# Kernel tuning notes

Measured on AMD Instinct MI355X. Metric: run time of the kernel, lower is better.

Reference implementation:

```python
import jax, jax.numpy as jnp
import numpy as np

N, E, HD, L, A = 50000, 600000, 128, 4, 50
EIN = 3 * HD + 1  # edge MLP input: [h_row, h_col, dist, lam_e]


def _p(k, shape, scale=0.05):
    return (scale * jax.random.normal(k, shape)).astype(jnp.float32)


def setup_inputs() -> dict:
    key = jax.random.key(0)
    ks = jax.random.split(key, 24)
    inp = {
        "z": jax.random.randint(ks[0], (N,), 0, A),
        "pos": jax.random.normal(ks[1], (N, 3), dtype=jnp.float32),
        "edge_index": jax.random.randint(ks[2], (2, E), 0, N),
        "lam": jax.random.uniform(ks[3], (), dtype=jnp.float32),
        "atom_embed": _p(ks[4], (A, HD), 1.0),
        "lam_w": _p(ks[5], (1, HD)),
        "lam_b": _p(ks[6], (HD,)),
        "edge_w1": _p(ks[7], (L, EIN, HD)),
        "edge_b1": jnp.zeros((L, HD), jnp.float32),
        "edge_w2": _p(ks[8], (L, HD, HD)),
        "edge_b2": jnp.zeros((L, HD), jnp.float32),
        "node_w1": _p(ks[9], (L, 2 * HD, HD)),
        "node_b1": jnp.zeros((L, HD), jnp.float32),
        "node_w2": _p(ks[10], (L, HD, HD)),
        "node_b2": jnp.zeros((L, HD), jnp.float32),
        "ln_g": jnp.ones((L, HD), jnp.float32),
        "ln_b": jnp.zeros((L, HD), jnp.float32),
        "head_w1": _p(ks[11], (HD, HD)),
        "head_b1": jnp.zeros((HD,), jnp.float32),
        "head_w2": _p(ks[12], (HD, 1)),
        "head_b2": jnp.zeros((1,), jnp.float32),
    }
    return inp


def _layernorm(x, g, b, eps=1e-5):
    mu = jnp.mean(x, -1, keepdims=True)
    var = jnp.mean(jnp.square(x - mu), -1, keepdims=True)
    return (x - mu) * jax.lax.rsqrt(var + eps) * g + b


def reference(z, pos, edge_index, lam, atom_embed, lam_w, lam_b,
              edge_w1, edge_b1, edge_w2, edge_b2,
              node_w1, node_b1, node_w2, node_b2, ln_g, ln_b,
              head_w1, head_b1, head_w2, head_b2):
    h = atom_embed[z]                                  # [N, HD]
    # lambda_embed(lam.expand(N,1)): same vector for every node
    lam_vec = lam * lam_w[0] + lam_b                    # [HD]
    lam_feat = jnp.broadcast_to(lam_vec, (h.shape[0], HD))
    h = h + lam_feat
    row, col = edge_index[0], edge_index[1]
    diff = pos[row] - pos[col]                          # [E, 3] (constant over layers)
    dist = jnp.sqrt(jnp.sum(diff * diff, -1, keepdims=True) + 1e-8)  # [E,1]
    lam_e = lam_feat[row]                               # [E, HD]
    for i in range(L):
        ein = jnp.concatenate([h[row], h[col], dist, lam_e], -1)      # [E, 3*HD+1]
        m = jax.nn.silu(ein @ edge_w1[i] + edge_b1[i])
        m = jax.nn.silu(m @ edge_w2[i] + edge_b2[i])                  # [E, HD]
        agg = jnp.zeros_like(h).at[row].add(m)                        # scatter-add
        u = jax.nn.silu(jnp.concatenate([h, agg], -1) @ node_w1[i] + node_b1[i])
        u = u @ node_w2[i] + node_b2[i]
        h = _layernorm(h + u, ln_g[i], ln_b[i])
    pooled = jnp.mean(h, 0, keepdims=True)              # [1, HD]
    out = jax.nn.silu(pooled @ head_w1 + head_b1) @ head_w2 + head_b2  # [1, 1]
    return out
```

## Files before the change

kernel.cpp:

```cpp
#include <hip/hip_runtime.h>
#include <cstdint>
#include <cstddef>

#define HD 128
#define NLAYER 4
#define EINDIM 385

typedef _Float16 f16x8 __attribute__((ext_vector_type(8)));
typedef _Float16 f16x4 __attribute__((ext_vector_type(4)));
typedef float f32x4 __attribute__((ext_vector_type(4)));

__device__ __forceinline__ float silu_f(float x) {
    float e = __expf(-x);
    return x * __builtin_amdgcn_rcpf(1.f + e);
}

__device__ __forceinline__ void lds_barrier() {
    asm volatile("s_waitcnt lgkmcnt(0)" ::: "memory");
    __builtin_amdgcn_s_barrier();
}

__global__ __launch_bounds__(128) void k_init(const float* __restrict__ lam_p,
                                              const float* __restrict__ lam_w,
                                              const float* __restrict__ lam_b,
                                              const float* __restrict__ edge_w1,
                                              const float* __restrict__ edge_b1,
                                              float* __restrict__ lam_vec,
                                              float* __restrict__ c1) {
    __shared__ float sl[HD];
    const int j = threadIdx.x;
    const int l = blockIdx.x;
    float lam = lam_p[0];
    float v = lam * lam_w[j] + lam_b[j];
    sl[j] = v;
    if (l == 0) lam_vec[j] = v;
    __syncthreads();
    float acc = edge_b1[l * HD + j];
    const float* w = edge_w1 + ((size_t)l * EINDIM + 257) * HD + j;
#pragma unroll 8
    for (int k = 0; k < HD; k++) acc = fmaf(sl[k], w[(size_t)k * HD], acc);
    c1[l * HD + j] = acc;
}

__global__ void k_prep(const float* __restrict__ ew1, const float* __restrict__ ew2,
                       const float* __restrict__ nw1, const float* __restrict__ nw2,
                       _Float16* __restrict__ W1te, _Float16* __restrict__ W2te,
                       _Float16* __restrict__ W1tn, _Float16* __restrict__ W2tn,
                       float* __restrict__ wd) {
    int t = blockIdx.x * 256 + threadIdx.x;
    if (t < NLAYER * 128 * 256) {
        int l = t >> 15, r = t & 32767, j = r >> 8, k = r & 255;
        W1te[t] = (_Float16)ew1[((size_t)l * EINDIM + k) * HD + j];
        return;
    }
    t -= NLAYER * 128 * 256;
    if (t < NLAYER * 128 * 256) {
        int l = t >> 15, r = t & 32767, j = r >> 8, k = r & 255;
        W1tn[t] = (_Float16)nw1[((size_t)l * 256 + k) * HD + j];
        return;
    }
    t -= NLAYER * 128 * 256;
    if (t < NLAYER * 128 * 128) {
        int l = t >> 14, r = t & 16383, j = r >> 7, k = r & 127;
        W2te[t] = (_Float16)ew2[((size_t)l * 128 + k) * HD + j];
        return;
    }
    t -= NLAYER * 128 * 128;
    if (t < NLAYER * 128 * 128) {
        int l = t >> 14, r = t & 16383, j = r >> 7, k = r & 127;
        W2tn[t] = (_Float16)nw2[((size_t)l * 128 + k) * HD + j];
        return;
    }
    t -= NLAYER * 128 * 128;
    if (t < NLAYER * 128) {
        int l = t >> 7, j = t & 127;
        wd[t] = ew1[((size_t)l * EINDIM + 256) * HD + j];
    }
}

__global__ void k_embed(const int* __restrict__ z,
                        const float* __restrict__ atom_embed,
                        const float* __restrict__ lam_vec,
                        float* __restrict__ h, _Float16* __restrict__ hh, int n4) {
    int i = blockIdx.x * 256 + threadIdx.x;
    if (i >= n4) return;
    int n = i >> 5, q = i & 31;
    int a = z[n];
    float4 e = *(const float4*)&atom_embed[(size_t)a * HD + q * 4];
    float4 lv = *(const float4*)&lam_vec[q * 4];
    e.x += lv.x; e.y += lv.y; e.z += lv.z; e.w += lv.w;
    *(float4*)&h[(size_t)n * HD + q * 4] = e;
    f16x4 hv;
    hv[0] = (_Float16)e.x; hv[1] = (_Float16)e.y;
    hv[2] = (_Float16)e.z; hv[3] = (_Float16)e.w;
    *(f16x4*)&hh[(size_t)n * HD + q * 4] = hv;
}

__global__ void k_zero(float4* __restrict__ p, int n4) {
    for (int i = blockIdx.x * 256 + threadIdx.x; i < n4; i += gridDim.x * 256)
        p[i] = make_float4(0.f, 0.f, 0.f, 0.f);
}

__global__ void k_hist(const int* __restrict__ ei, int* __restrict__ deg, int E) {
    int e = blockIdx.x * 256 + threadIdx.x;
    if (e < E) atomicAdd(&deg[ei[e]], 1);
}

__global__ __launch_bounds__(1024) void k_scan(const int* __restrict__ deg,
                                               int* __restrict__ cursor, int N) {
    __shared__ int part[1024];
    int t = threadIdx.x;
    int chunk = (N + 1023) >> 10;
    int s0 = t * chunk, s1 = s0 + chunk;
    if (s1 > N) s1 = N;
    int s = 0;
    for (int i = s0; i < s1; i++) s += deg[i];
    part[t] = s;
    __syncthreads();
    for (int d = 1; d < 1024; d <<= 1) {
        int v = (t >= d) ? part[t - d] : 0;
        __syncthreads();
        part[t] += v;
        __syncthreads();
    }
    int base = (t == 0) ? 0 : part[t - 1];
    for (int i = s0; i < s1; i++) {
        cursor[i] = base;
        base += deg[i];
    }
}

__global__ void k_scatter(const int* __restrict__ ei, int* __restrict__ cursor,
                          int* __restrict__ perm, int E) {
    int e = blockIdx.x * 256 + threadIdx.x;
    if (e < E) {
        int p = atomicAdd(&cursor[ei[e]], 1);
        perm[p] = e;
    }
}

__global__ void k_apply(const int* __restrict__ perm, const int* __restrict__ ei,
                        const float* __restrict__ pos,
                        int* __restrict__ rowS, int* __restrict__ colS,
                        float* __restrict__ distS, int E, int Epad) {
    int i = blockIdx.x * 256 + threadIdx.x;
    if (i >= Epad) return;
    if (i < E) {
        int e = perm[i];
        int r = ei[e], c = ei[E + e];
        rowS[i] = r; colS[i] = c;
        float dx = pos[r * 3 + 0] - pos[c * 3 + 0];
        float dy = pos[r * 3 + 1] - pos[c * 3 + 1];
        float dz = pos[r * 3 + 2] - pos[c * 3 + 2];
        distS[i] = sqrtf(dx * dx + dy * dy + dz * dz + 1e-8f);
    } else {
        rowS[i] = -1; colS[i] = 0; distS[i] = 0.f;
    }
}

__global__ void k_mask(const int* __restrict__ rowS,
                       unsigned long long* __restrict__ maskBuf, int Epad) {
    int i = blockIdx.x * 256 + threadIdx.x;
    if (i >= Epad) return;
    bool pred = (i + 1 >= Epad) ? true : (rowS[i] != rowS[i + 1]);
    unsigned long long m = __ballot(pred);
    if ((i & 63) == 0) maskBuf[i >> 6] = m;
}

__global__ __launch_bounds__(512, 4) void k_edge_mfma(
    const _Float16* __restrict__ hh,
    const int* __restrict__ rowS, const int* __restrict__ colS,
    const float* __restrict__ distS,
    const unsigned long long* __restrict__ maskBuf,
    int Epad, int ntiles, int tpb,
    const _Float16* __restrict__ W1t,
    const _Float16* __restrict__ W2t,
    const float* __restrict__ wd, const float* __restrict__ c1,
    const float* __restrict__ b2,
    float* __restrict__ agg) {
    __shared__ __align__(16) _Float16 shA[64 * 264];
    __shared__ __align__(16) _Float16 shM[64 * 136];
    __shared__ int shRow2[2][64];
    __shared__ float shD2[2][64];
    __shared__ float shWd[HD], shC1[HD], shB2[HD];

    const int tid = threadIdx.x;
    const int w = tid >> 6, l = tid & 63;
    const int lg = l >> 4, lr = l & 15;
    const int col = w * 16 + lr;

    f16x8 w1f[8], w2f[4];
#pragma unroll
    for (int s = 0; s < 8; s++)
        w1f[s] = *(const f16x8*)(W1t + (size_t)col * 256 + s * 32 + lg * 8);
#pragma unroll
    for (int s = 0; s < 4; s++)
        w2f[s] = *(const f16x8*)(W2t + (size_t)col * 128 + s * 32 + lg * 8);
    if (tid < 128) { shWd[tid] = wd[tid]; shC1[tid] = c1[tid]; }
    else if (tid < 256) shB2[tid - 128] = b2[tid - 128];

    const int t0 = blockIdx.x * tpb;
    int t1 = t0 + tpb; if (t1 > ntiles) t1 = ntiles;
    if (t0 >= t1) return;

    f16x8 vA[4];
    int rv = -1; float dv = 0.f;

    {
        const int e0 = t0 * 64;
        if (tid < 64) { rv = rowS[e0 + tid]; dv = distS[e0 + tid]; }
#pragma unroll
        for (int it = 0; it < 4; it++) {
            int flat = tid + it * 512;
            int e = flat >> 5, c = flat & 31;
            int idx = (c < 16) ? rowS[e0 + e] : colS[e0 + e];
            if (idx < 0) idx = 0;
            int cc = (c < 16) ? c : (c - 16);
            vA[it] = *(const f16x8*)(hh + (size_t)idx * HD + cc * 8);
        }
    }
    __syncthreads();

    for (int t = t0; t < t1; t++) {
        const int pb = t & 1;
        const unsigned long long bmCur = maskBuf[t];
        const unsigned long long bmPrev = (t > 0) ? maskBuf[t - 1] : ~0ull;

#pragma unroll
        for (int it = 0; it < 4; it++) {
            int flat = tid + it * 512;
            int e = flat >> 5, c = flat & 31;
            *(f16x8*)&shA[e * 264 + c * 8] = vA[it];
        }
        if (tid < 64) { shRow2[pb][tid] = rv; shD2[pb][tid] = dv; }

        {
            int tn = t + 1; if (tn > ntiles - 1) tn = ntiles - 1;
            const int e0n = tn * 64;
#pragma unroll
            for (int it = 0; it < 4; it++) {
                int flat = tid + it * 512;
                int e = flat >> 5, c = flat & 31;
                int idx = (c < 16) ? rowS[e0n + e] : colS[e0n + e];
                if (idx < 0) idx = 0;
                int cc = (c < 16) ? c : (c - 16);
                vA[it] = *(const f16x8*)(hh + (size_t)idx * HD + cc * 8);
            }
            if (tid < 64) { rv = rowS[e0n + tid]; dv = distS[e0n + tid]; }
        }

        lds_barrier();

        f32x4 acc[4];
#pragma unroll
        for (int rf = 0; rf < 4; rf++) acc[rf] = (f32x4){0.f, 0.f, 0.f, 0.f};

#pragma unroll
        for (int s = 0; s < 8; s++) {
#pragma unroll
            for (int rf = 0; rf < 4; rf++) {
                f16x8 a = *(const f16x8*)&shA[(rf * 16 + lr) * 264 + s * 32 + lg * 8];
                acc[rf] = __builtin_amdgcn_mfma_f32_16x16x32_f16(a, w1f[s], acc[rf], 0, 0, 0);
            }
        }
#pragma unroll
        for (int rf = 0; rf < 4; rf++) {
#pragma unroll
            for (int r = 0; r < 4; r++) {
                int row = rf * 16 + lg * 4 + r;
                float x = acc[rf][r] + shD2[pb][row] * shWd[col] + shC1[col];
                shM[row * 136 + col] = (_Float16)silu_f(x);
            }
            acc[rf] = (f32x4){0.f, 0.f, 0.f, 0.f};
        }
        lds_barrier();

#pragma unroll
        for (int s = 0; s < 4; s++) {
#pragma unroll
            for (int rf = 0; rf < 4; rf++) {
                f16x8 a = *(const f16x8*)&shM[(rf * 16 + lr) * 136 + s * 32 + lg * 8];
                acc[rf] = __builtin_amdgcn_mfma_f32_16x16x32_f16(a, w2f[s], acc[rf], 0, 0, 0);
            }
        }
        lds_barrier();

#pragma unroll
        for (int rf = 0; rf < 4; rf++) {
#pragma unroll
            for (int r = 0; r < 4; r++) {
                int row = rf * 16 + lg * 4 + r;
                shM[row * 136 + col] = (_Float16)silu_f(acc[rf][r] + shB2[col]);
            }
        }
        lds_barrier();

        {
            const int scol = tid & 127, quarter = tid >> 7;
            const int i0 = quarter << 4;
            const unsigned int mh = (unsigned int)(bmCur >> i0) & 0xFFFFu;
            bool open = (quarter == 0) ? !((bmPrev >> 63) & 1ull)
                                       : !((bmCur >> (i0 - 1)) & 1ull);
            float s = 0.f;
#pragma unroll
            for (int ib = 0; ib < 4; ib++) {
                const int i = i0 + ib * 4;
                float v0 = (float)shM[(i + 0) * 136 + scol];
                float v1 = (float)shM[(i + 1) * 136 + scol];
                float v2 = (float)shM[(i + 2) * 136 + scol];
                float v3 = (float)shM[(i + 3) * 136 + scol];
#pragma unroll
                for (int q = 0; q < 4; q++) {
                    s += (q == 0) ? v0 : (q == 1) ? v1 : (q == 2) ? v2 : v3;
                    if (mh & (1u << (ib * 4 + q))) {
                        int rc = shRow2[pb][i + q];
                        if (rc >= 0) {
                            if (open) atomicAdd(&agg[(size_t)rc * HD + scol], s);
                            else      agg[(size_t)rc * HD + scol] = s;
                        }
                        s = 0.f;
                        open = false;
                    }
                }
            }
            if (!((mh >> 15) & 1u)) {
                int rc = shRow2[pb][i0 + 15];
                if (rc >= 0) atomicAdd(&agg[(size_t)rc * HD + scol], s);
            }
        }
    }
}

__global__ __launch_bounds__(256, 3) void k_node_mfma(
    const _Float16* __restrict__ hh_in, float* __restrict__ agg, int N,
    int ntiles, int tpb,
    const _Float16* __restrict__ W1t,
    const _Float16* __restrict__ W2t,
    const float* __restrict__ b1, const float* __restrict__ b2,
    const float* __restrict__ lng, const float* __restrict__ lnb,
    float* __restrict__ h, _Float16* __restrict__ hh_out) {
    __shared__ __align__(16) _Float16 shA[64 * 264];
    __shared__ __align__(16) _Float16 shM[64 * 136];
    __shared__ float shB1[HD], shB2[HD], shG[HD], shBt[HD];

    const int tid = threadIdx.x;
    const int w = tid >> 6, l = tid & 63;
    const int lg = l >> 4, lr = l & 15;

    f16x8 w1f[2][8], w2f[2][4];
#pragma unroll
    for (int cf = 0; cf < 2; cf++) {
        const int col = w * 32 + cf * 16 + lr;
#pragma unroll
        for (int s = 0; s < 8; s++)
            w1f[cf][s] = *(const f16x8*)(W1t + (size_t)col * 256 + s * 32 + lg * 8);
#pragma unroll
        for (int s = 0; s < 4; s++)
            w2f[cf][s] = *(const f16x8*)(W2t + (size_t)col * 128 + s * 32 + lg * 8);
    }
    if (tid < 128) { shB1[tid] = b1[tid]; shB2[tid] = b2[tid]; }
    else { shG[tid - 128] = lng[tid - 128]; shBt[tid - 128] = lnb[tid - 128]; }
    __syncthreads();

    int t1 = blockIdx.x * tpb + tpb;
    if (t1 > ntiles) t1 = ntiles;
    for (int t = blockIdx.x * tpb; t < t1; t++) {
        const int n0 = t * 64;

#pragma unroll
        for (int it = 0; it < 8; it++) {
            int flat = tid + it * 256;
            int e = flat >> 5, c = flat & 31;
            int n = n0 + e;
            f16x8 v = {};
            if (n < N) {
                if (c < 16) {
                    v = *(const f16x8*)(hh_in + (size_t)n * HD + c * 8);
                } else {
                    float* s = agg + (size_t)n * HD + (c - 16) * 8;
                    float4 v0 = *(const float4*)s;
                    float4 v1 = *(const float4*)(s + 4);
                    v[0] = (_Float16)v0.x; v[1] = (_Float16)v0.y;
                    v[2] = (_Float16)v0.z; v[3] = (_Float16)v0.w;
                    v[4] = (_Float16)v1.x; v[5] = (_Float16)v1.y;
                    v[6] = (_Float16)v1.z; v[7] = (_Float16)v1.w;
                    float4 z4 = make_float4(0.f, 0.f, 0.f, 0.f);
                    *(float4*)s = z4;
                    *(float4*)(s + 4) = z4;
                }
            }
            *(f16x8*)&shA[e * 264 + c * 8] = v;
        }
        lds_barrier();

        f32x4 acc[4][2];
#pragma unroll
        for (int rf = 0; rf < 4; rf++)
#pragma unroll
            for (int cf = 0; cf < 2; cf++) acc[rf][cf] = (f32x4){0.f, 0.f, 0.f, 0.f};

#pragma unroll
        for (int s = 0; s < 8; s++) {
#pragma unroll
            for (int rf = 0; rf < 4; rf++) {
                f16x8 a = *(const f16x8*)&shA[(rf * 16 + lr) * 264 + s * 32 + lg * 8];
                acc[rf][0] = __builtin_amdgcn_mfma_f32_16x16x32_f16(a, w1f[0][s], acc[rf][0], 0, 0, 0);
                acc[rf][1] = __builtin_amdgcn_mfma_f32_16x16x32_f16(a, w1f[1][s], acc[rf][1], 0, 0, 0);
            }
        }
#pragma unroll
        for (int rf = 0; rf < 4; rf++)
#pragma unroll
            for (int cf = 0; cf < 2; cf++) {
                const int col = w * 32 + cf * 16 + lr;
#pragma unroll
                for (int r = 0; r < 4; r++) {
                    int row = rf * 16 + lg * 4 + r;
                    shM[row * 136 + col] = (_Float16)silu_f(acc[rf][cf][r] + shB1[col]);
                }
            }
        lds_barrier();

        f32x4 acc2[4][2];
#pragma unroll
        for (int rf = 0; rf < 4; rf++)
#pragma unroll
            for (int cf = 0; cf < 2; cf++) acc2[rf][cf] = (f32x4){0.f, 0.f, 0.f, 0.f};

#pragma unroll
        for (int s = 0; s < 4; s++) {
#pragma unroll
            for (int rf = 0; rf < 4; rf++) {
                f16x8 a = *(const f16x8*)&shM[(rf * 16 + lr) * 136 + s * 32 + lg * 8];
                acc2[rf][0] = __builtin_amdgcn_mfma_f32_16x16x32_f16(a, w2f[0][s], acc2[rf][0], 0, 0, 0);
                acc2[rf][1] = __builtin_amdgcn_mfma_f32_16x16x32_f16(a, w2f[1][s], acc2[rf][1], 0, 0, 0);
            }
        }
        lds_barrier();

#pragma unroll
        for (int rf = 0; rf < 4; rf++)
#pragma unroll
            for (int cf = 0; cf < 2; cf++) {
                const int col = w * 32 + cf * 16 + lr;
#pragma unroll
                for (int r = 0; r < 4; r++) {
                    int row = rf * 16 + lg * 4 + r;
                    shM[row * 136 + col] = (_Float16)(acc2[rf][cf][r] + shB2[col]);
                }
            }
        lds_barrier();

        {
            int row = tid >> 2, q = tid & 3, n = n0 + row;
            float s = 0.f, ss = 0.f;
            if (n < N) {
#pragma unroll
                for (int j = 0; j < 8; j++) {
                    float4 hv = *(const float4*)&h[(size_t)n * HD + q * 32 + j * 4];
                    int cb = q * 32 + j * 4;
                    f16x4 uv = *(const f16x4*)&shM[row * 136 + cb];
                    float x0 = (float)uv[0] + hv.x;
                    float x1 = (float)uv[1] + hv.y;
                    float x2 = (float)uv[2] + hv.z;
                    float x3 = (float)uv[3] + hv.w;
                    s += x0 + x1 + x2 + x3;
                    ss += x0 * x0 + x1 * x1 + x2 * x2 + x3 * x3;
                }
            }
            s += __shfl_xor(s, 1);  s += __shfl_xor(s, 2);
            ss += __shfl_xor(ss, 1); ss += __shfl_xor(ss, 2);
            float mean = s * (1.f / 128.f);
            float var = ss * (1.f / 128.f) - mean * mean;
            float rstd = rsqrtf(var + 1e-5f);
            if (n < N) {
#pragma unroll
                for (int j = 0; j < 8; j++) {
                    float4 hv = *(const float4*)&h[(size_t)n * HD + q * 32 + j * 4];
                    int cb = q * 32 + j * 4;
                    f16x4 uv = *(const f16x4*)&shM[row * 136 + cb];
                    float4 y;
                    y.x = ((float)uv[0] + hv.x - mean) * rstd * shG[cb + 0] + shBt[cb + 0];
                    y.y = ((float)uv[1] + hv.y - mean) * rstd * shG[cb + 1] + shBt[cb + 1];
                    y.z = ((float)uv[2] + hv.z - mean) * rstd * shG[cb + 2] + shBt[cb + 2];
                    y.w = ((float)uv[3] + hv.w - mean) * rstd * shG[cb + 3] + shBt[cb + 3];
                    *(float4*)&h[(size_t)n * HD + cb] = y;
                    f16x4 yh;
                    yh[0] = (_Float16)y.x; yh[1] = (_Float16)y.y;
                    yh[2] = (_Float16)y.z; yh[3] = (_Float16)y.w;
                    *(f16x4*)&hh_out[(size_t)n * HD + cb] = yh;
                }
            }
        }
    }
}

__global__ __launch_bounds__(256) void k_pool1(const float* __restrict__ h,
                                               float* __restrict__ partial,
                                               int N, int RPB) {
    int bk = blockIdx.x, t = threadIdx.x;
    int j = t & 127, half = t >> 7;
    float s = 0.f;
    int rend = (bk + 1) * RPB; if (rend > N) rend = N;
    for (int r = bk * RPB + half; r < rend; r += 2) s += h[(size_t)r * HD + j];
    __shared__ float sh[256];
    sh[t] = s;
    __syncthreads();
    if (t < 128) partial[bk * HD + j] = sh[t] + sh[t + 128];
}

__global__ __launch_bounds__(128) void k_head(const float* __restrict__ partial,
                                              int nPart, int N,
                                              const float* __restrict__ hw1,
                                              const float* __restrict__ hb1,
                                              const float* __restrict__ hw2,
                                              const float* __restrict__ hb2,
                                              float* __restrict__ out) {
    __shared__ float pooled[HD];
    __shared__ float t1[HD];
    int j = threadIdx.x;
    double s = 0.0;
    for (int bk = 0; bk < nPart; bk++) s += (double)partial[bk * HD + j];
    pooled[j] = (float)(s / (double)N);
    __syncthreads();
    float acc = hb1[j];
    for (int k = 0; k < HD; k++) acc = fmaf(pooled[k], hw1[k * HD + j], acc);
    t1[j] = silu_f(acc) * hw2[j];
    __syncthreads();
    if (j < 64) t1[j] += t1[j + 64];
    __syncthreads();
    if (j < 64) {
        float v = t1[j];
#pragma unroll
        for (int o = 32; o > 0; o >>= 1) v += __shfl_xor(v, o);
        if (j == 0) out[0] = v + hb2[0];
    }
}

extern "C" void kernel_launch(void* const* d_in, const int* in_sizes, int n_in,
                              void* d_out, int out_size, void* d_ws, size_t ws_size,
                              hipStream_t stream) {
    const int* z      = (const int*)d_in[0];
    const float* pos  = (const float*)d_in[1];
    const int* ei     = (const int*)d_in[2];
    const float* lam  = (const float*)d_in[3];
    const float* aemb = (const float*)d_in[4];
    const float* lamw = (const float*)d_in[5];
    const float* lamb = (const float*)d_in[6];
    const float* ew1  = (const float*)d_in[7];
    const float* eb1  = (const float*)d_in[8];
    const float* ew2  = (const float*)d_in[9];
    const float* eb2  = (const float*)d_in[10];
    const float* nw1  = (const float*)d_in[11];
    const float* nb1  = (const float*)d_in[12];
    const float* nw2  = (const float*)d_in[13];
    const float* nb2  = (const float*)d_in[14];
    const float* lng  = (const float*)d_in[15];
    const float* lnb  = (const float*)d_in[16];
    const float* hw1  = (const float*)d_in[17];
    const float* hb1  = (const float*)d_in[18];
    const float* hw2  = (const float*)d_in[19];
    const float* hb2  = (const float*)d_in[20];

    const int N = in_sizes[0];
    const int E = in_sizes[2] / 2;
    const int etiles = (E + 63) / 64;
    const int Epad = etiles * 64;
    const int ntilesN = (N + 63) / 64;

    char* ws = (char*)d_ws;
    size_t off = 0;
    auto alloc = [&](size_t bytes) { void* p = ws + off; off += (bytes + 255) & ~(size_t)255; return p; };
    float* h        = (float*)alloc((size_t)N * HD * 4);
    float* agg      = (float*)alloc((size_t)N * HD * 4);
    _Float16* hh    = (_Float16*)alloc((size_t)N * HD * 2);
    int* deg        = (int*)alloc((size_t)N * 4);
    int* cursor     = (int*)alloc((size_t)N * 4);
    int* perm       = (int*)alloc((size_t)E * 4);
    int* rowS       = (int*)alloc((size_t)Epad * 4);
    int* colS       = (int*)alloc((size_t)Epad * 4);
    float* distS    = (float*)alloc((size_t)Epad * 4);
    unsigned long long* maskBuf = (unsigned long long*)alloc((size_t)etiles * 8);
    float* lamv     = (float*)alloc(HD * 4);
    float* c1       = (float*)alloc(NLAYER * HD * 4);
    float* wd       = (float*)alloc(NLAYER * HD * 4);
    float* part     = (float*)alloc(256 * HD * 4);
    _Float16* W1te  = (_Float16*)alloc((size_t)NLAYER * 128 * 256 * 2);
    _Float16* W1tn  = (_Float16*)alloc((size_t)NLAYER * 128 * 256 * 2);
    _Float16* W2te  = (_Float16*)alloc((size_t)NLAYER * 128 * 128 * 2);
    _Float16* W2tn  = (_Float16*)alloc((size_t)NLAYER * 128 * 128 * 2);

    k_init<<<NLAYER, 128, 0, stream>>>(lam, lamw, lamb, ew1, eb1, lamv, c1);
    int prepTot = NLAYER * 128 * 256 * 2 + NLAYER * 128 * 128 * 2 + NLAYER * 128;
    k_prep<<<(prepTot + 255) / 256, 256, 0, stream>>>(ew1, ew2, nw1, nw2,
                                                      W1te, W2te, W1tn, W2tn, wd);
    int n4 = N * 32;
    k_embed<<<(n4 + 255) / 256, 256, 0, stream>>>(z, aemb, lamv, h, hh, n4);

    k_zero<<<64, 256, 0, stream>>>((float4*)deg, (N + 3) / 4);
    k_hist<<<(E + 255) / 256, 256, 0, stream>>>(ei, deg, E);
    k_scan<<<1, 1024, 0, stream>>>(deg, cursor, N);
    k_scatter<<<(E + 255) / 256, 256, 0, stream>>>(ei, cursor, perm, E);
    k_apply<<<(Epad + 255) / 256, 256, 0, stream>>>(perm, ei, pos, rowS, colS, distS, E, Epad);
    k_mask<<<(Epad + 255) / 256, 256, 0, stream>>>(rowS, maskBuf, Epad);

    int zero4 = N * (HD / 4);
    k_zero<<<2048, 256, 0, stream>>>((float4*)agg, zero4);

    const int egrid = (etiles < 512) ? etiles : 512;
    const int etpb = (etiles + egrid - 1) / egrid;
    const int ngrid = (ntilesN + 1) / 2;
    for (int l = 0; l < NLAYER; l++) {
        k_edge_mfma<<<egrid, 512, 0, stream>>>(hh, rowS, colS, distS, maskBuf,
            Epad, etiles, etpb,
            W1te + (size_t)l * 128 * 256, W2te + (size_t)l * 128 * 128,
            wd + l * HD, c1 + l * HD, eb2 + l * HD, agg);
        k_node_mfma<<<ngrid, 256, 0, stream>>>(hh, agg, N, ntilesN, 2,
            W1tn + (size_t)l * 128 * 256, W2tn + (size_t)l * 128 * 128,
            nb1 + l * HD, nb2 + l * HD, lng + l * HD, lnb + l * HD, h, hh);
    }
    int RPB = (N + 255) / 256;
    k_pool1<<<256, 256, 0, stream>>>(h, part, N, RPB);
    k_head<<<1, 128, 0, stream>>>(part, 256, N, hw1, hb1, hw2, hb2, (float*)d_out);
}
```

Baseline: 958.9 us.

## Factor first edge-MLP layer into per-node projections gathered per edge

The first edge linear layer is split by linearity: each node's h is projected once through the row and col halves of W1 in a new per-node MFMA kernel (P, Q), and the edge kernel gathers P[row]+Q[col] and adds the dist and lambda terms before SiLU. This replaces the per-edge 256-wide GEMM with a 128-wide node GEMM over far fewer nodes, and removes one LDS staging buffer and barrier from the edge loop. It adds an extra kernel launch per layer and an extra write/read of two N×128 half buffers, and the pre-activation sum is now done in fp16-rounded pieces, which slightly changes precision.

```diff
diff --git a/kernel.cpp b/kernel.cpp
--- a/kernel.cpp
+++ b/kernel.cpp
@@ -26,7 +26,8 @@
                                               const float* __restrict__ edge_w1,
                                               const float* __restrict__ edge_b1,
                                               float* __restrict__ lam_vec,
-                                              float* __restrict__ c1) {
+                                              float* __restrict__ c1,
+                                              _Float16* __restrict__ c1h) {
     __shared__ float sl[HD];
     const int j = threadIdx.x;
     const int l = blockIdx.x;
@@ -40,13 +41,14 @@
 #pragma unroll 8
     for (int k = 0; k < HD; k++) acc = fmaf(sl[k], w[(size_t)k * HD], acc);
     c1[l * HD + j] = acc;
+    c1h[l * HD + j] = (_Float16)acc;
 }
 
 __global__ void k_prep(const float* __restrict__ ew1, const float* __restrict__ ew2,
                        const float* __restrict__ nw1, const float* __restrict__ nw2,
                        _Float16* __restrict__ W1te, _Float16* __restrict__ W2te,
                        _Float16* __restrict__ W1tn, _Float16* __restrict__ W2tn,
-                       float* __restrict__ wd) {
+                       float* __restrict__ wd, _Float16* __restrict__ wdh) {
     int t = blockIdx.x * 256 + threadIdx.x;
     if (t < NLAYER * 128 * 256) {
         int l = t >> 15, r = t & 32767, j = r >> 8, k = r & 255;
@@ -74,7 +76,9 @@
     t -= NLAYER * 128 * 128;
     if (t < NLAYER * 128) {
         int l = t >> 7, j = t & 127;
-        wd[t] = ew1[((size_t)l * EINDIM + 256) * HD + j];
+        float v = ew1[((size_t)l * EINDIM + 256) * HD + j];
+        wd[t] = v;
+        wdh[t] = (_Float16)v;
     }
 }
 
@@ -167,86 +171,143 @@
     if ((i & 63) == 0) maskBuf[i >> 6] = m;
 }
 
+__global__ __launch_bounds__(512, 4) void k_pq(
+    const _Float16* __restrict__ hh, int N,
+    const _Float16* __restrict__ W1t,
+    _Float16* __restrict__ Ph, _Float16* __restrict__ Qh) {
+    __shared__ __align__(16) _Float16 shH[64 * 136];
+    const int tid = threadIdx.x;
+    const int w = tid >> 6, l = tid & 63;
+    const int lg = l >> 4, lr = l & 15;
+    const int col = w * 16 + lr;
+
+    f16x8 w1a[4], w1b[4];
+#pragma unroll
+    for (int s = 0; s < 4; s++) {
+        w1a[s] = *(const f16x8*)(W1t + (size_t)col * 256 + s * 32 + lg * 8);
+        w1b[s] = *(const f16x8*)(W1t + (size_t)col * 256 + 128 + s * 32 + lg * 8);
+    }
+    const int n0 = blockIdx.x * 64;
+#pragma unroll
+    for (int it = 0; it < 2; it++) {
+        int flat = tid + it * 512;
+        int e = flat >> 4, c = flat & 15;
+        int n = n0 + e;
+        f16x8 v = {};
+        if (n < N) v = *(const f16x8*)(hh + (size_t)n * HD + c * 8);
+        *(f16x8*)&shH[e * 136 + c * 8] = v;
+    }
+    __syncthreads();
+
+    f32x4 aP[4], aQ[4];
+#pragma unroll
+    for (int rf = 0; rf < 4; rf++) { aP[rf] = (f32x4){0,0,0,0}; aQ[rf] = (f32x4){0,0,0,0}; }
+#pragma unroll
+    for (int s = 0; s < 4; s++) {
+#pragma unroll
+        for (int rf = 0; rf < 4; rf++) {
+            f16x8 a = *(const f16x8*)&shH[(rf * 16 + lr) * 136 + s * 32 + lg * 8];
+            aP[rf] = __builtin_amdgcn_mfma_f32_16x16x32_f16(a, w1a[s], aP[rf], 0, 0, 0);
+            aQ[rf] = __builtin_amdgcn_mfma_f32_16x16x32_f16(a, w1b[s], aQ[rf], 0, 0, 0);
+        }
+    }
+#pragma unroll
+    for (int rf = 0; rf < 4; rf++) {
+#pragma unroll
+        for (int r = 0; r < 4; r++) {
+            int n = n0 + rf * 16 + lg * 4 + r;
+            if (n < N) {
+                Ph[(size_t)n * HD + col] = (_Float16)aP[rf][r];
+                Qh[(size_t)n * HD + col] = (_Float16)aQ[rf][r];
+            }
+        }
+    }
+}
+
 __global__ __launch_bounds__(512, 4) void k_edge_mfma(
-    const _Float16* __restrict__ hh,
+    const _Float16* __restrict__ Ph, const _Float16* __restrict__ Qh,
     const int* __restrict__ rowS, const int* __restrict__ colS,
     const float* __restrict__ distS,
     const unsigned long long* __restrict__ maskBuf,
     int Epad, int ntiles, int tpb,
-    const _Float16* __restrict__ W1t,
     const _Float16* __restrict__ W2t,
-    const float* __restrict__ wd, const float* __restrict__ c1,
+    const _Float16* __restrict__ wdh, const _Float16* __restrict__ c1h,
     const float* __restrict__ b2,
     float* __restrict__ agg) {
-    __shared__ __align__(16) _Float16 shA[64 * 264];
     __shared__ __align__(16) _Float16 shM[64 * 136];
     __shared__ int shRow2[2][64];
-    __shared__ float shD2[2][64];
-    __shared__ float shWd[HD], shC1[HD], shB2[HD];
 
     const int tid = threadIdx.x;
     const int w = tid >> 6, l = tid & 63;
     const int lg = l >> 4, lr = l & 15;
     const int col = w * 16 + lr;
-
-    f16x8 w1f[8], w2f[4];
-#pragma unroll
-    for (int s = 0; s < 8; s++)
-        w1f[s] = *(const f16x8*)(W1t + (size_t)col * 256 + s * 32 + lg * 8);
+    const int cc = tid & 15;
+
+    f16x8 w2f[4];
 #pragma unroll
     for (int s = 0; s < 4; s++)
         w2f[s] = *(const f16x8*)(W2t + (size_t)col * 128 + s * 32 + lg * 8);
-    if (tid < 128) { shWd[tid] = wd[tid]; shC1[tid] = c1[tid]; }
-    else if (tid < 256) shB2[tid - 128] = b2[tid - 128];
+    const f16x8 wd8 = *(const f16x8*)(wdh + cc * 8);
+    const f16x8 c18 = *(const f16x8*)(c1h + cc * 8);
+    const float b2v = b2[col];
 
     const int t0 = blockIdx.x * tpb;
     int t1 = t0 + tpb; if (t1 > ntiles) t1 = ntiles;
     if (t0 >= t1) return;
 
-    f16x8 vA[4];
-    int rv = -1; float dv = 0.f;
+    f16x8 vP[2], vQ[2];
+    float dva[2];
+    int rv = -1;
 
     {
         const int e0 = t0 * 64;
-        if (tid < 64) { rv = rowS[e0 + tid]; dv = distS[e0 + tid]; }
-#pragma unroll
-        for (int it = 0; it < 4; it++) {
-            int flat = tid + it * 512;
-            int e = flat >> 5, c = flat & 31;
-            int idx = (c < 16) ? rowS[e0 + e] : colS[e0 + e];
-            if (idx < 0) idx = 0;
-            int cc = (c < 16) ? c : (c - 16);
-            vA[it] = *(const f16x8*)(hh + (size_t)idx * HD + cc * 8);
-        }
-    }
-    __syncthreads();
+        if (tid < 64) rv = rowS[e0 + tid];
+#pragma unroll
+        for (int it = 0; it < 2; it++) {
+            int e = (tid + it * 512) >> 4;
+            int r_ = rowS[e0 + e], q_ = colS[e0 + e];
+            if (r_ < 0) r_ = 0;
+            vP[it] = *(const f16x8*)(Ph + (size_t)r_ * HD + cc * 8);
+            vQ[it] = *(const f16x8*)(Qh + (size_t)q_ * HD + cc * 8);
+            dva[it] = distS[e0 + e];
+        }
+    }
 
     for (int t = t0; t < t1; t++) {
         const int pb = t & 1;
         const unsigned long long bmCur = maskBuf[t];
         const unsigned long long bmPrev = (t > 0) ? maskBuf[t - 1] : ~0ull;
 
-#pragma unroll
-        for (int it = 0; it < 4; it++) {
-            int flat = tid + it * 512;
-            int e = flat >> 5, c = flat & 31;
-            *(f16x8*)&shA[e * 264 + c * 8] = vA[it];
-        }
-        if (tid < 64) { shRow2[pb][tid] = rv; shD2[pb][tid] = dv; }
+        lds_barrier();
+
+#pragma unroll
+        for (int it = 0; it < 2; it++) {
+            int e = (tid + it * 512) >> 4;
+            float d = dva[it];
+            f16x8 mv;
+#pragma unroll
+            for (int j = 0; j < 8; j++) {
+                float x = (float)vP[it][j] + (float)vQ[it][j]
+                        + d * (float)wd8[j] + (float)c18[j];
+                mv[j] = (_Float16)silu_f(x);
+            }
+            *(f16x8*)&shM[e * 136 + cc * 8] = mv;
+        }
+        if (tid < 64) shRow2[pb][tid] = rv;
 
         {
             int tn = t + 1; if (tn > ntiles - 1) tn = ntiles - 1;
             const int e0n = tn * 64;
 #pragma unroll
-            for (int it = 0; it < 4; it++) {
-                int flat = tid + it * 512;
-                int e = flat >> 5, c = flat & 31;
-                int idx = (c < 16) ? rowS[e0n + e] : colS[e0n + e];
-                if (idx < 0) idx = 0;
-                int cc = (c < 16) ? c : (c - 16);
-                vA[it] = *(const f16x8*)(hh + (size_t)idx * HD + cc * 8);
-            }
-            if (tid < 64) { rv = rowS[e0n + tid]; dv = distS[e0n + tid]; }
+            for (int it = 0; it < 2; it++) {
+                int e = (tid + it * 512) >> 4;
+                int r_ = rowS[e0n + e], q_ = colS[e0n + e];
+                if (r_ < 0) r_ = 0;
+                vP[it] = *(const f16x8*)(Ph + (size_t)r_ * HD + cc * 8);
+                vQ[it] = *(const f16x8*)(Qh + (size_t)q_ * HD + cc * 8);
+                dva[it] = distS[e0n + e];
+            }
+            if (tid < 64) rv = rowS[e0n + tid];
         }
 
         lds_barrier();
@@ -254,26 +315,6 @@
         f32x4 acc[4];
 #pragma unroll
         for (int rf = 0; rf < 4; rf++) acc[rf] = (f32x4){0.f, 0.f, 0.f, 0.f};
-
-#pragma unroll
-        for (int s = 0; s < 8; s++) {
-#pragma unroll
-            for (int rf = 0; rf < 4; rf++) {
-                f16x8 a = *(const f16x8*)&shA[(rf * 16 + lr) * 264 + s * 32 + lg * 8];
-                acc[rf] = __builtin_amdgcn_mfma_f32_16x16x32_f16(a, w1f[s], acc[rf], 0, 0, 0);
-            }
-        }
-#pragma unroll
-        for (int rf = 0; rf < 4; rf++) {
-#pragma unroll
-            for (int r = 0; r < 4; r++) {
-                int row = rf * 16 + lg * 4 + r;
-                float x = acc[rf][r] + shD2[pb][row] * shWd[col] + shC1[col];
-                shM[row * 136 + col] = (_Float16)silu_f(x);
-            }
-            acc[rf] = (f32x4){0.f, 0.f, 0.f, 0.f};
-        }
-        lds_barrier();
 
 #pragma unroll
         for (int s = 0; s < 4; s++) {
@@ -290,7 +331,7 @@
 #pragma unroll
             for (int r = 0; r < 4; r++) {
                 int row = rf * 16 + lg * 4 + r;
-                shM[row * 136 + col] = (_Float16)silu_f(acc[rf][r] + shB2[col]);
+                shM[row * 136 + col] = (_Float16)silu_f(acc[rf][r] + b2v);
             }
         }
         lds_barrier();
@@ -574,6 +615,8 @@
     float* h        = (float*)alloc((size_t)N * HD * 4);
     float* agg      = (float*)alloc((size_t)N * HD * 4);
     _Float16* hh    = (_Float16*)alloc((size_t)N * HD * 2);
+    _Float16* Ph    = (_Float16*)alloc((size_t)N * HD * 2);
+    _Float16* Qh    = (_Float16*)alloc((size_t)N * HD * 2);
     int* deg        = (int*)alloc((size_t)N * 4);
     int* cursor     = (int*)alloc((size_t)N * 4);
     int* perm       = (int*)alloc((size_t)E * 4);
@@ -583,17 +626,19 @@
     unsigned long long* maskBuf = (unsigned long long*)alloc((size_t)etiles * 8);
     float* lamv     = (float*)alloc(HD * 4);
     float* c1       = (float*)alloc(NLAYER * HD * 4);
+    _Float16* c1h   = (_Float16*)alloc(NLAYER * HD * 2);
     float* wd       = (float*)alloc(NLAYER * HD * 4);
+    _Float16* wdh   = (_Float16*)alloc(NLAYER * HD * 2);
     float* part     = (float*)alloc(256 * HD * 4);
     _Float16* W1te  = (_Float16*)alloc((size_t)NLAYER * 128 * 256 * 2);
     _Float16* W1tn  = (_Float16*)alloc((size_t)NLAYER * 128 * 256 * 2);
     _Float16* W2te  = (_Float16*)alloc((size_t)NLAYER * 128 * 128 * 2);
     _Float16* W2tn  = (_Float16*)alloc((size_t)NLAYER * 128 * 128 * 2);
 
-    k_init<<<NLAYER, 128, 0, stream>>>(lam, lamw, lamb, ew1, eb1, lamv, c1);
+    k_init<<<NLAYER, 128, 0, stream>>>(lam, lamw, lamb, ew1, eb1, lamv, c1, c1h);
     int prepTot = NLAYER * 128 * 256 * 2 + NLAYER * 128 * 128 * 2 + NLAYER * 128;
     k_prep<<<(prepTot + 255) / 256, 256, 0, stream>>>(ew1, ew2, nw1, nw2,
-                                                      W1te, W2te, W1tn, W2tn, wd);
+                                                      W1te, W2te, W1tn, W2tn, wd, wdh);
     int n4 = N * 32;
     k_embed<<<(n4 + 255) / 256, 256, 0, stream>>>(z, aemb, lamv, h, hh, n4);
 
@@ -611,10 +656,11 @@
     const int etpb = (etiles + egrid - 1) / egrid;
     const int ngrid = (ntilesN + 1) / 2;
     for (int l = 0; l < NLAYER; l++) {
-        k_edge_mfma<<<egrid, 512, 0, stream>>>(hh, rowS, colS, distS, maskBuf,
+        k_pq<<<ntilesN, 512, 0, stream>>>(hh, N, W1te + (size_t)l * 128 * 256, Ph, Qh);
+        k_edge_mfma<<<egrid, 512, 0, stream>>>(Ph, Qh, rowS, colS, distS, maskBuf,
             Epad, etiles, etpb,
-            W1te + (size_t)l * 128 * 256, W2te + (size_t)l * 128 * 128,
-            wd + l * HD, c1 + l * HD, eb2 + l * HD, agg);
+            W2te + (size_t)l * 128 * 128, wdh + l * HD, c1h + l * HD,
+            eb2 + l * HD, agg);
         k_node_mfma<<<ngrid, 256, 0, stream>>>(hh, agg, N, ntilesN, 2,
             W1tn + (size_t)l * 128 * 256, W2tn + (size_t)l * 128 * 128,
             nb1 + l * HD, nb2 + l * HD, lng + l * HD, lnb + l * HD, h, hh);
```

New measurement: 873.2 us. 8.9% less time.
